# Performance work log

Hardware: AMD Instinct MI355X
Metric: run time of the kernel (lower is better)

The kernel has to match this reference:

```python
import jax, jax.numpy as jnp
import numpy as np

# Dims: img=64, Nslice=16, Ncoil=4, Nsingular=4, Necho=3, N_readout=32, Npoint=96
IMG = 64
NSLICE = 16
NCOIL = 4
NSING = 4
NECHO = 3
NRO = 32
NPT = 96


def setup_inputs() -> dict:
    key = jax.random.key(0)
    k = jax.random.split(key, 6)
    singulars = jax.random.normal(k[0], (IMG, IMG, NSLICE, NSING, NECHO, 2), jnp.float32)
    smap = jax.random.normal(k[1], (NCOIL, IMG, IMG, NSLICE, 2), jnp.float32)
    # k-space trajectory in radians, [-pi, pi)
    ktraj = (jax.random.uniform(k[2], (1, NRO, NPT, 2), jnp.float32) - 0.5) * (2.0 * np.pi)
    Ur_list = jax.random.normal(k[3], (1, NRO, NSING), jnp.float32)
    slice_bin_list = jax.random.randint(k[4], (NRO,), 0, NSLICE)
    dc = jax.random.uniform(k[5], (NPT,), jnp.float32)
    return {"singulars": singulars, "smap": smap, "ktraj": ktraj,
            "Ur_list": Ur_list, "slice_bin_list": slice_bin_list, "dc": dc}


def reference(singulars, smap, ktraj, Ur_list, slice_bin_list, dc):
    # dc is density compensation; used only in the original (custom) backward.
    X, Y, Z, Ns, Ne, _ = singulars.shape
    C = smap.shape[0]
    sc = singulars[..., 0] + 1j * singulars[..., 1]              # [X,Y,Z,Ns,Ne] c64
    sc = jnp.transpose(sc, (3, 4, 0, 1, 2)).reshape(Ns * Ne, 1, X, Y, Z)  # [S,1,X,Y,Z]
    # sign flip on odd slices (fftshift trick along kz)
    sign = jnp.where(jnp.arange(Z) % 2 == 1, -1.0, 1.0).astype(jnp.float32)
    sc = sc * sign
    sm = smap[..., 0] + 1j * smap[..., 1]                        # [C,X,Y,Z]
    sc = sc * sm[None]                                            # [S,C,X,Y,Z]
    scf = jnp.fft.fft(sc, axis=-1)                                # FFT along slice dim

    kt = ktraj[0]                                                 # [R,P,2]
    ur = Ur_list[0]                                               # [R,Ns]
    # gather the slice image for each readout
    img_g = scf[..., slice_bin_list]                              # [S,C,X,Y,R]

    xs = (jnp.arange(X) - X // 2).astype(jnp.float32)
    ys = (jnp.arange(Y) - Y // 2).astype(jnp.float32)
    # exact (type-2) NUFFT, separable phase: exp(-i(w0*x + w1*y)), centered grid
    ex = jnp.exp(-1j * kt[..., 0, None] * xs)                     # [R,P,X]
    ey = jnp.exp(-1j * kt[..., 1, None] * ys)                     # [R,P,Y]
    t1 = jnp.einsum('scxyr,rpx->scrpy', img_g, ex)                # [S,C,R,P,Y]
    nuf = jnp.einsum('scrpy,rpy->scrp', t1, ey)                   # [S,C,R,P]
    nuf = nuf.reshape(Ns, Ne, C, kt.shape[0], kt.shape[1])        # [Ns,Ne,C,R,P]
    # singular-vector weighted sum: [P,C,R,Ne]
    out = jnp.einsum('necrp,rn->pcre', nuf, ur.astype(nuf.dtype))
    # view_as_real
    return jnp.stack([out.real, out.imag], axis=-1)               # [P,C,R,Ne,2]
```

## Files before the change

### kernel.cpp

```cpp
#include <hip/hip_runtime.h>
#include <math.h>

#define IMG 64
#define NPIX 4096
#define NSLICE 16
#define NCOIL 4
#define NSING 4
#define NECHO 3
#define NRO 32
#define NPT 96
#define NEC 12

typedef float v2f __attribute__((ext_vector_type(2)));

#define EXG2_F2 (NRO * 33 * NPT)

__global__ __launch_bounds__(256) void precompute_imgw(
    const float2* __restrict__ sing,
    const float2* __restrict__ smap,
    const float*  __restrict__ ur,
    const int*    __restrict__ zb,
    const float*  __restrict__ kt,
    float2* __restrict__ ex2,
    float2* __restrict__ imgw)
{
  __shared__ float2 sc_sh[4 * 192];
  __shared__ float2 sm_sh[4 * 64];
  __shared__ float2 f_sh[4 * 48 * 16];
  __shared__ float  ur_sh[128];
  __shared__ int    zb_sh[32];

  const int t   = threadIdx.x;
  const int px0 = blockIdx.x * 4;

  if (blockIdx.x < 396) {
    int g = blockIdx.x * 256 + t;
    int p = g % 96;
    int k = (g / 96) % 33;
    int r = g / (96 * 33);
    float w0 = kt[(r * 96 + p) * 2];
    float ang = (k == 0) ? (32.0f * w0) : (-(float)k * w0);
    float s_, c_;
    __sincosf(ang, &s_, &c_);
    ex2[g] = make_float2(c_, s_);
  }

  for (int j = t; j < 768; j += 256) sc_sh[j] = sing[px0 * 192 + j];
  {
    int c = t >> 6, pxl = (t >> 4) & 3, z = t & 15;
    sm_sh[pxl * 64 + c * 16 + z] = smap[c * 65536 + (px0 + pxl) * 16 + z];
  }
  if (t < 128) ur_sh[t] = ur[t];
  if (t < 32)  zb_sh[t] = zb[t];
  __syncthreads();

  const int pxl = t >> 6, lane = t & 63;
  const int s = lane >> 2, c = lane & 3;

  const float wr[16] = { 1.f,  0.92387953f,  0.70710678f,  0.38268343f,
                         0.f, -0.38268343f, -0.70710678f, -0.92387953f,
                        -1.f, -0.92387953f, -0.70710678f, -0.38268343f,
                         0.f,  0.38268343f,  0.70710678f,  0.92387953f };
  const float wi[16] = { 0.f, -0.38268343f, -0.70710678f, -0.92387953f,
                        -1.f, -0.92387953f, -0.70710678f, -0.38268343f,
                         0.f,  0.38268343f,  0.70710678f,  0.92387953f,
                         1.f,  0.92387953f,  0.70710678f,  0.92387953f };
  const float wi_fix[16] = { 0.f, -0.38268343f, -0.70710678f, -0.92387953f,
                        -1.f, -0.92387953f, -0.70710678f, -0.38268343f,
                         0.f,  0.38268343f,  0.70710678f,  0.92387953f,
                         1.f,  0.92387953f,  0.70710678f,  0.38268343f };

  if (lane < 48) {
    float br[16], bi[16];
    #pragma unroll
    for (int z = 0; z < 16; ++z) {
      float2 a = sc_sh[pxl * 192 + z * 12 + s];
      float2 m = sm_sh[pxl * 64 + c * 16 + z];
      float sg = (z & 1) ? -1.f : 1.f;
      br[z] = sg * (a.x * m.x - a.y * m.y);
      bi[z] = sg * (a.x * m.y + a.y * m.x);
    }
    float Er[8], Ei[8], Or[8], Oi[8];
    #pragma unroll
    for (int k = 0; k < 8; ++k) {
      float er = 0.f, ei = 0.f, pr = 0.f, pi = 0.f;
      #pragma unroll
      for (int m = 0; m < 8; ++m) {
        const int idx = (2 * k * m) & 15;
        er = fmaf(br[2*m],    wr[idx], er); er = fmaf(-bi[2*m],   wi_fix[idx], er);
        ei = fmaf(br[2*m],    wi_fix[idx], ei); ei = fmaf( bi[2*m],   wr[idx], ei);
        pr = fmaf(br[2*m+1],  wr[idx], pr); pr = fmaf(-bi[2*m+1], wi_fix[idx], pr);
        pi = fmaf(br[2*m+1],  wi_fix[idx], pi); pi = fmaf( bi[2*m+1], wr[idx], pi);
      }
      Er[k] = er; Ei[k] = ei; Or[k] = pr; Oi[k] = pi;
    }
    float2* frow = &f_sh[(pxl * 48 + s * 4 + c) * 16];
    #pragma unroll
    for (int k = 0; k < 8; ++k) {
      float tr = Or[k] * wr[k] - Oi[k] * wi_fix[k];
      float ti = Or[k] * wi_fix[k] + Oi[k] * wr[k];
      frow[k]     = make_float2(Er[k] + tr, Ei[k] + ti);
      frow[k + 8] = make_float2(Er[k] - tr, Ei[k] - ti);
    }
  }
  __syncthreads();

  for (int j = t; j < 1536; j += 256) {
    int rc  = j >> 2;
    int pl  = j & 3;
    int r   = rc / 12, ec = rc - r * 12;
    int e   = ec >> 2, cc = ec & 3;
    int kz  = zb_sh[r];
    float vr = 0.f, vi = 0.f;
    #pragma unroll
    for (int n = 0; n < 4; ++n) {
      float u  = ur_sh[r * 4 + n];
      float2 f = f_sh[(pl * 48 + (n * 3 + e) * 4 + cc) * 16 + kz];
      vr = fmaf(u, f.x, vr);
      vi = fmaf(u, f.y, vi);
    }
    imgw[rc * 4096 + px0 + pl] = make_float2(vr, vi);
  }
}

__global__ __launch_bounds__(256, 3) void nufft_points(
    const float*  __restrict__ kt,
    const float2* __restrict__ ex2,
    const float2* __restrict__ imgw,
    float2* __restrict__ out)
{
  __shared__ float2 w_sh[4096];
  __shared__ float2 ex_sh[33 * 48];

  const int bid = blockIdx.x;
  const int r   = bid & 31;
  const int ec  = (bid >> 5) % 12;
  const int ps  = bid / 384;
  const int e   = ec >> 2, c = ec & 3;
  const int t    = threadIdx.x;
  const int lane = t & 63;
  const int p0l  = (t >> 6) * 12;
  const int p0   = ps * 48 + p0l;

  {
    const float4* wsrc = (const float4*)(imgw + (r * 12 + ec) * 4096);
    float4* wdst = (float4*)w_sh;
    #pragma unroll
    for (int j = 0; j < 8; ++j) wdst[t + j * 256] = wsrc[t + j * 256];
  }
  {
    const float2* esrc = ex2 + r * (33 * 96) + ps * 48;
    for (int idx = t; idx < 33 * 48; idx += 256) {
      int k = idx / 48, pl = idx - k * 48;
      ex_sh[idx] = esrc[k * 96 + pl];
    }
  }
  __syncthreads();

  float2 wa[8], wb[8];
  #pragma unroll
  for (int j = 0; j < 8; ++j) {
    int idx = t + j * 256;
    if (idx < 1984) {
      int k = 1 + (idx >> 6), y = idx & 63;
      wa[j] = w_sh[(32 + k) * 64 + y];
      wb[j] = w_sh[(32 - k) * 64 + y];
    }
  }
  __syncthreads();
  #pragma unroll
  for (int j = 0; j < 8; ++j) {
    int idx = t + j * 256;
    if (idx < 1984) {
      int k = 1 + (idx >> 6), y = idx & 63;
      w_sh[(32 + k) * 64 + y] = make_float2(wa[j].x + wb[j].x, wa[j].y + wb[j].y);
      w_sh[(32 - k) * 64 + y] = make_float2(-(wa[j].y - wb[j].y), wa[j].x - wb[j].x);
    }
  }
  __syncthreads();

  v2f acc[12];
  {
    float2 w0v = w_sh[lane];
    float2 w32 = w_sh[32 * 64 + lane];
    #pragma unroll
    for (int pp = 0; pp < 12; ++pp) {
      float2 e0 = ex_sh[p0l + pp];
      acc[pp].x = w32.x + w0v.x * e0.x - w0v.y * e0.y;
      acc[pp].y = w32.y + w0v.x * e0.y + w0v.y * e0.x;
    }
  }

  #pragma unroll 2
  for (int k = 1; k < 32; ++k) {
    v2f sxy = *(const v2f*)&w_sh[(32 + k) * 64 + lane];
    v2f dyx = *(const v2f*)&w_sh[(32 - k) * 64 + lane];
    const float2* ekb = &ex_sh[k * 48 + p0l];
    #pragma unroll
    for (int pp = 0; pp < 12; ++pp) {
      float2 ev = ekb[pp];
      acc[pp] = __builtin_elementwise_fma(sxy, (v2f)(ev.x), acc[pp]);
      acc[pp] = __builtin_elementwise_fma(dyx, (v2f)(ev.y), acc[pp]);
    }
  }

  const float yy = (float)(lane - 32);
  #pragma unroll
  for (int pp = 0; pp < 12; ++pp) {
    const int p = p0 + pp;
    float w1 = kt[(r * 96 + p) * 2 + 1];
    float es, ecos;
    __sincosf(-w1 * yy, &es, &ecos);
    float vr = acc[pp].x * ecos - acc[pp].y * es;
    float vi = acc[pp].x * es  + acc[pp].y * ecos;
    #pragma unroll
    for (int off = 32; off; off >>= 1) {
      vr += __shfl_xor(vr, off);
      vi += __shfl_xor(vi, off);
    }
    if (lane == 0) out[((p * 4 + c) * 32 + r) * 3 + e] = make_float2(vr, vi);
  }
}

extern "C" void kernel_launch(void* const* d_in, const int* in_sizes, int n_in,
                              void* d_out, int out_size, void* d_ws, size_t ws_size,
                              hipStream_t stream) {
  const float2* sing  = (const float2*)d_in[0];
  const float2* smap  = (const float2*)d_in[1];
  const float*  ktraj = (const float*)d_in[2];
  const float*  ur    = (const float*)d_in[3];
  const int*    zbin  = (const int*)d_in[4];

  float2* ex2  = (float2*)d_ws;
  float2* imgw = ex2 + EXG2_F2;
  float2* out  = (float2*)d_out;

  precompute_imgw<<<NPIX / 4, 256, 0, stream>>>(sing, smap, ur, zbin, ktraj, ex2, imgw);
  nufft_points<<<NRO * NEC * 2, 256, 0, stream>>>(ktraj, ex2, imgw, out);
}
```

Measured before the change: 97.93 us.

## Fold w symmetrization into global load and use transposed butterfly reduction

The nufft_points kernel now computes the sum/difference pairs directly while loading imgw from global memory and stores them as packed float4 in shared memory. This removes two block barriers and the shared-memory read-modify-write pass. The 12 per-point wave reductions are replaced by a recursive-halving butterfly that reduces 12 values with far fewer shuffles, and each result is written by a different lane. The ktraj loads are hoisted to the kernel start and ex reads are vectorized to float4. In exchange the index logic is more complex and register pressure rises slightly.

```diff
diff --git a/kernel.cpp b/kernel.cpp
--- a/kernel.cpp
+++ b/kernel.cpp
@@ -61,10 +61,6 @@
                          0.f, -0.38268343f, -0.70710678f, -0.92387953f,
                         -1.f, -0.92387953f, -0.70710678f, -0.38268343f,
                          0.f,  0.38268343f,  0.70710678f,  0.92387953f };
-  const float wi[16] = { 0.f, -0.38268343f, -0.70710678f, -0.92387953f,
-                        -1.f, -0.92387953f, -0.70710678f, -0.38268343f,
-                         0.f,  0.38268343f,  0.70710678f,  0.92387953f,
-                         1.f,  0.92387953f,  0.70710678f,  0.92387953f };
   const float wi_fix[16] = { 0.f, -0.38268343f, -0.70710678f, -0.92387953f,
                         -1.f, -0.92387953f, -0.70710678f, -0.38268343f,
                          0.f,  0.38268343f,  0.70710678f,  0.92387953f,
@@ -129,8 +125,10 @@
     const float2* __restrict__ imgw,
     float2* __restrict__ out)
 {
-  __shared__ float2 w_sh[4096];
-  __shared__ float2 ex_sh[33 * 48];
+  __shared__ float4 w2_sh[31 * 64];
+  __shared__ float2 w0_sh[64];
+  __shared__ float2 w32_sh[64];
+  __shared__ __align__(16) float2 ex_sh[33 * 48];
 
   const int bid = blockIdx.x;
   const int r   = bid & 31;
@@ -142,11 +140,23 @@
   const int p0l  = (t >> 6) * 12;
   const int p0   = ps * 48 + p0l;
 
-  {
-    const float4* wsrc = (const float4*)(imgw + (r * 12 + ec) * 4096);
-    float4* wdst = (float4*)w_sh;
-    #pragma unroll
-    for (int j = 0; j < 8; ++j) wdst[t + j * 256] = wsrc[t + j * 256];
+  float w1v[12];
+  #pragma unroll
+  for (int pp = 0; pp < 12; ++pp) w1v[pp] = kt[(r * 96 + p0 + pp) * 2 + 1];
+
+  const float2* __restrict__ wsrc = imgw + (r * 12 + ec) * 4096;
+
+  if (t < 128) {
+    int which = t >> 6, y = t & 63;
+    float2 v = wsrc[which * 32 * 64 + y];
+    if (which == 0) w0_sh[y] = v; else w32_sh[y] = v;
+  }
+  for (int idx = t; idx < 31 * 64; idx += 256) {
+    int k = 1 + (idx >> 6), y = idx & 63;
+    float2 wa = wsrc[(32 + k) * 64 + y];
+    float2 wb = wsrc[(32 - k) * 64 + y];
+    w2_sh[idx] = make_float4(wa.x + wb.x, wa.y + wb.y,
+                             -(wa.y - wb.y), wa.x - wb.x);
   }
   {
     const float2* esrc = ex2 + r * (33 * 96) + ps * 48;
@@ -157,68 +167,80 @@
   }
   __syncthreads();
 
-  float2 wa[8], wb[8];
-  #pragma unroll
-  for (int j = 0; j < 8; ++j) {
-    int idx = t + j * 256;
-    if (idx < 1984) {
-      int k = 1 + (idx >> 6), y = idx & 63;
-      wa[j] = w_sh[(32 + k) * 64 + y];
-      wb[j] = w_sh[(32 - k) * 64 + y];
-    }
-  }
-  __syncthreads();
-  #pragma unroll
-  for (int j = 0; j < 8; ++j) {
-    int idx = t + j * 256;
-    if (idx < 1984) {
-      int k = 1 + (idx >> 6), y = idx & 63;
-      w_sh[(32 + k) * 64 + y] = make_float2(wa[j].x + wb[j].x, wa[j].y + wb[j].y);
-      w_sh[(32 - k) * 64 + y] = make_float2(-(wa[j].y - wb[j].y), wa[j].x - wb[j].x);
-    }
-  }
-  __syncthreads();
-
   v2f acc[12];
   {
-    float2 w0v = w_sh[lane];
-    float2 w32 = w_sh[32 * 64 + lane];
-    #pragma unroll
-    for (int pp = 0; pp < 12; ++pp) {
-      float2 e0 = ex_sh[p0l + pp];
-      acc[pp].x = w32.x + w0v.x * e0.x - w0v.y * e0.y;
-      acc[pp].y = w32.y + w0v.x * e0.y + w0v.y * e0.x;
+    float2 w0v = w0_sh[lane];
+    float2 w32 = w32_sh[lane];
+    const float4* e40 = (const float4*)(ex_sh + p0l);
+    #pragma unroll
+    for (int pq = 0; pq < 6; ++pq) {
+      float4 e2 = e40[pq];
+      acc[2*pq].x   = w32.x + w0v.x * e2.x - w0v.y * e2.y;
+      acc[2*pq].y   = w32.y + w0v.x * e2.y + w0v.y * e2.x;
+      acc[2*pq+1].x = w32.x + w0v.x * e2.z - w0v.y * e2.w;
+      acc[2*pq+1].y = w32.y + w0v.x * e2.w + w0v.y * e2.z;
     }
   }
 
   #pragma unroll 2
   for (int k = 1; k < 32; ++k) {
-    v2f sxy = *(const v2f*)&w_sh[(32 + k) * 64 + lane];
-    v2f dyx = *(const v2f*)&w_sh[(32 - k) * 64 + lane];
-    const float2* ekb = &ex_sh[k * 48 + p0l];
-    #pragma unroll
-    for (int pp = 0; pp < 12; ++pp) {
-      float2 ev = ekb[pp];
-      acc[pp] = __builtin_elementwise_fma(sxy, (v2f)(ev.x), acc[pp]);
-      acc[pp] = __builtin_elementwise_fma(dyx, (v2f)(ev.y), acc[pp]);
+    float4 wv = w2_sh[(k - 1) * 64 + lane];
+    v2f sxy = { wv.x, wv.y };
+    v2f dyx = { wv.z, wv.w };
+    const float4* e4 = (const float4*)(ex_sh + k * 48 + p0l);
+    #pragma unroll
+    for (int pq = 0; pq < 6; ++pq) {
+      float4 e2 = e4[pq];
+      acc[2*pq]   = __builtin_elementwise_fma(sxy, (v2f)(e2.x), acc[2*pq]);
+      acc[2*pq]   = __builtin_elementwise_fma(dyx, (v2f)(e2.y), acc[2*pq]);
+      acc[2*pq+1] = __builtin_elementwise_fma(sxy, (v2f)(e2.z), acc[2*pq+1]);
+      acc[2*pq+1] = __builtin_elementwise_fma(dyx, (v2f)(e2.w), acc[2*pq+1]);
     }
   }
 
   const float yy = (float)(lane - 32);
   #pragma unroll
   for (int pp = 0; pp < 12; ++pp) {
+    float es, ec_;
+    __sincosf(-w1v[pp] * yy, &es, &ec_);
+    v2f tv;
+    tv.x = acc[pp].x * ec_ - acc[pp].y * es;
+    tv.y = acc[pp].x * es  + acc[pp].y * ec_;
+    acc[pp] = tv;
+  }
+
+  const int b5 = (lane >> 5) & 1, b4 = (lane >> 4) & 1;
+  const int b3 = (lane >> 3) & 1, b2 = (lane >> 2) & 1;
+
+#define RPAIR(OUT, A, B, BIT, OFF) do {            \
+    v2f x_ = (BIT) ? (B) : (A);                    \
+    v2f y_ = (BIT) ? (A) : (B);                    \
+    v2f s_;                                        \
+    s_.x = __shfl_xor(y_.x, OFF);                  \
+    s_.y = __shfl_xor(y_.y, OFF);                  \
+    OUT = x_ + s_;                                 \
+  } while (0)
+
+  v2f w6[6];
+  #pragma unroll
+  for (int i = 0; i < 6; ++i) RPAIR(w6[i], acc[2*i], acc[2*i+1], b5, 32);
+  v2f X0, X1, X2;
+  RPAIR(X0, w6[0], w6[1], b4, 16);
+  RPAIR(X1, w6[2], w6[3], b4, 16);
+  RPAIR(X2, w6[4], w6[5], b4, 16);
+  v2f Y0, Y1;
+  RPAIR(Y0, X0, X1, b3, 8);
+  { v2f s_; s_.x = __shfl_xor(X2.x, 8); s_.y = __shfl_xor(X2.y, 8); Y1 = X2 + s_; }
+  v2f Z;
+  RPAIR(Z, Y0, Y1, b2, 4);
+  { v2f s_; s_.x = __shfl_xor(Z.x, 2); s_.y = __shfl_xor(Z.y, 2); Z = Z + s_; }
+  { v2f s_; s_.x = __shfl_xor(Z.x, 1); s_.y = __shfl_xor(Z.y, 1); Z = Z + s_; }
+#undef RPAIR
+
+  const int pp = b2 ? (8 + 2 * b4 + b5) : (4 * b3 + 2 * b4 + b5);
+  if (((lane & 3) == 0) && (b2 == 0 || b3 == 0)) {
     const int p = p0 + pp;
-    float w1 = kt[(r * 96 + p) * 2 + 1];
-    float es, ecos;
-    __sincosf(-w1 * yy, &es, &ecos);
-    float vr = acc[pp].x * ecos - acc[pp].y * es;
-    float vi = acc[pp].x * es  + acc[pp].y * ecos;
-    #pragma unroll
-    for (int off = 32; off; off >>= 1) {
-      vr += __shfl_xor(vr, off);
-      vi += __shfl_xor(vi, off);
-    }
-    if (lane == 0) out[((p * 4 + c) * 32 + r) * 3 + e] = make_float2(vr, vi);
+    out[((p * 4 + c) * 32 + r) * 3 + e] = make_float2(Z.x, Z.y);
   }
 }
 
```

New measurement: 95.88 us. -2.1%, faster.
